# Optimization experiments

Hardware: AMD Instinct MI355X
Metric: run time of the kernel (lower is better)

Reference implementation:

```python
import jax, jax.numpy as jnp
import numpy as np

VOCAB = 32000
H = 256        # d_model
L = 4096       # l_max
N = 64         # SSM state size (S4 default)
CH = 1         # channels
BATCH = 8
PAD = 0        # pad_token_id
DT_MIN, DT_MAX = 0.001, 0.1


def setup_inputs() -> dict:
    key = jax.random.key(0)
    ks = jax.random.split(key, 8)
    input_ids = jax.random.randint(ks[0], (BATCH, L), 0, VOCAB)
    embedding = (jax.random.normal(ks[1], (VOCAB, H), dtype=jnp.float32) * 0.02).at[PAD].set(0.0)
    # S4D-Lin style initialization
    log_dt = jnp.log(DT_MIN) + jax.random.uniform(ks[2], (H,), dtype=jnp.float32) * (np.log(DT_MAX) - np.log(DT_MIN))
    A_log_re = jnp.full((H, N), np.log(0.5), dtype=jnp.float32)          # A_real = -exp(A_log_re)
    A_im = jnp.broadcast_to(np.pi * jnp.arange(N, dtype=jnp.float32), (H, N)).copy()
    B_re = jnp.ones((H, N), dtype=jnp.float32)
    B_im = jnp.zeros((H, N), dtype=jnp.float32)
    # bidirectional => 2*CH output channels for C
    C_re = jax.random.normal(ks[3], (2 * CH, H, N), dtype=jnp.float32) * (0.5 ** 0.5)
    C_im = jax.random.normal(ks[4], (2 * CH, H, N), dtype=jnp.float32) * (0.5 ** 0.5)
    D = jax.random.normal(ks[5], (CH, H), dtype=jnp.float32)
    W_out = jax.random.normal(ks[6], (2 * H, CH * H), dtype=jnp.float32) / np.sqrt(CH * H)
    b_out = jnp.zeros((2 * H,), dtype=jnp.float32)
    return {"input_ids": input_ids, "embedding": embedding, "log_dt": log_dt,
            "A_log_re": A_log_re, "A_im": A_im, "B_re": B_re, "B_im": B_im,
            "C_re": C_re, "C_im": C_im, "D": D, "W_out": W_out, "b_out": b_out}


def _s4_forward(input_ids, embedding, log_dt, A_log_re, A_im, B_re, B_im, C_re, C_im, D, W_out, b_out):
    u = embedding[input_ids]                 # (B, L, H) embedding lookup
    u = jnp.swapaxes(u, 1, 2)                # (B, H, L) transposed=True
    dt = jnp.exp(log_dt)                     # (H,)
    A = -jnp.exp(A_log_re) + 1j * A_im       # (H, N) Hurwitz diagonal SSM
    dtA = dt[:, None] * A                    # (H, N)
    dA = jnp.exp(dtA)                        # discrete A (ZOH)
    dB = (B_re + 1j * B_im) * (dA - 1.0) / A # discrete B (ZOH), (H, N)
    Cc = C_re + 1j * C_im                    # (2*CH, H, N)
    # Vandermonde kernel: K[c,h,l] = 2*Re(sum_n C[c,h,n] dB[h,n] exp(dtA[h,n]*l))
    pos = jnp.arange(L, dtype=jnp.float32)
    vand = jnp.exp(dtA[:, :, None] * pos)    # (H, N, L) complex
    K = 2.0 * jnp.einsum('chn,hn,hnl->chl', Cc, dB, vand).real  # (2*CH, H, L)
    # bidirectional: causal kernel + flipped anti-causal kernel, conv length 2L
    k0, k1 = K[:CH], K[CH:]
    k = jnp.pad(k0, ((0, 0), (0, 0), (0, L))) + jnp.pad(k1[..., ::-1], ((0, 0), (0, 0), (L, 0)))
    k_f = jnp.fft.rfft(k, n=2 * L)           # (CH, H, L+1)
    u_f = jnp.fft.rfft(u, n=2 * L)           # (B, H, L+1)
    y = jnp.fft.irfft(u_f[:, None] * k_f[None], n=2 * L)[..., :L]  # (B, CH, H, L)
    y = y + u[:, None, :, :] * D[None, :, :, None]                 # skip connection
    y = y.reshape(u.shape[0], CH * H, L)
    y = jax.nn.gelu(y, approximate=False)
    z = jnp.einsum('oi,bil->bol', W_out, y) + b_out[None, :, None]  # (B, 2H, L)
    y = z[:, :H] * jax.nn.sigmoid(z[:, H:])                          # GLU
    y = jnp.swapaxes(y, 1, 2)                # (B, L, H)
    return y[:, -1]                           # pool='last' -> (B, H)


def reference(input_ids, embedding, log_dt, A_log_re, A_im, B_re, B_im, C_re, C_im, D, W_out, b_out):
    return _s4_forward(input_ids, embedding, log_dt, A_log_re, A_im, B_re, B_im, C_re, C_im, D, W_out, b_out)
```

## Files before the change

kernel.cpp:

```cpp
#include <hip/hip_runtime.h>
#include <math.h>

#define HH 256
#define NN 64
#define LL 4096
#define BB 8
#define CC 8
#define LC (LL / CC)
#define GG 16
#define HN (HH * NN)

typedef __attribute__((ext_vector_type(2))) float pf2;
typedef __attribute__((ext_vector_type(16))) float f16v;
typedef const __attribute__((address_space(4))) f16v* cf16p;


__global__ __launch_bounds__(512) void frontend_kernel(
    const int* __restrict__ ids, const float* __restrict__ emb,
    const float* __restrict__ log_dt, const float* __restrict__ A_log_re,
    const float* __restrict__ A_im, const float* __restrict__ B_re,
    const float* __restrict__ B_im, const float* __restrict__ C_re,
    const float* __restrict__ C_im,
    float2* __restrict__ dAo, float2* __restrict__ wo, float2* __restrict__ pw,
    float* __restrict__ u_ws) {
    int t = threadIdx.x;
    if (blockIdx.x < BB * 64) {
        __shared__ int ids_s[64];
        __shared__ float tb[2][64][65];
        int b = blockIdx.x >> 6;
        int tile = blockIdx.x & 63;
        int w = t >> 6;
        int lane = t & 63;
        int rq = lane >> 4;
        int k = lane & 15;
        if (t < 64) ids_s[t] = ids[b * LL + tile * 64 + t];
        __syncthreads();
        {
            int r0 = w * 8 + rq;
            float4 v0 = *(const float4*)(emb + (long)ids_s[r0] * HH + 4 * k);
            float4 v1 = *(const float4*)(emb + (long)ids_s[r0 + 4] * HH + 4 * k);
            tb[0][r0][4 * k + 0] = v0.x;
            tb[0][r0][4 * k + 1] = v0.y;
            tb[0][r0][4 * k + 2] = v0.z;
            tb[0][r0][4 * k + 3] = v0.w;
            tb[0][r0 + 4][4 * k + 0] = v1.x;
            tb[0][r0 + 4][4 * k + 1] = v1.y;
            tb[0][r0 + 4][4 * k + 2] = v1.z;
            tb[0][r0 + 4][4 * k + 3] = v1.w;
        }
        __syncthreads();
        #pragma unroll
        for (int c4 = 0; c4 < 4; ++c4) {
            int cur = c4 & 1;
            float4 v0, v1;
            if (c4 < 3) {
                int r0 = w * 8 + rq;
                v0 = *(const float4*)(emb + (long)ids_s[r0] * HH +
                                      (c4 + 1) * 64 + 4 * k);
                v1 = *(const float4*)(emb + (long)ids_s[r0 + 4] * HH +
                                      (c4 + 1) * 64 + 4 * k);
            }
            #pragma unroll
            for (int it = 0; it < 2; ++it) {
                int hq = w * 8 + it * 4 + rq;
                int s0 = 4 * k;
                float4 o;
                o.x = tb[cur][s0 + 0][hq];
                o.y = tb[cur][s0 + 1][hq];
                o.z = tb[cur][s0 + 2][hq];
                o.w = tb[cur][s0 + 3][hq];
                *(float4*)(u_ws + ((long)(b * HH + c4 * 64 + hq)) * LL +
                           tile * 64 + s0) = o;
            }
            if (c4 < 3) {
                int r0 = w * 8 + rq;
                tb[cur ^ 1][r0][4 * k + 0] = v0.x;
                tb[cur ^ 1][r0][4 * k + 1] = v0.y;
                tb[cur ^ 1][r0][4 * k + 2] = v0.z;
                tb[cur ^ 1][r0][4 * k + 3] = v0.w;
                tb[cur ^ 1][r0 + 4][4 * k + 0] = v1.x;
                tb[cur ^ 1][r0 + 4][4 * k + 1] = v1.y;
                tb[cur ^ 1][r0 + 4][4 * k + 2] = v1.z;
                tb[cur ^ 1][r0 + 4][4 * k + 3] = v1.w;
            }
            __syncthreads();
        }
    } else {
        int idx = (blockIdx.x - BB * 64) * 512 + t;
        int h = idx >> 6;
        float dt = expf(log_dt[h]);
        float Are = -expf(A_log_re[idx]);
        float Aim = A_im[idx];
        float ea = expf(dt * Are);
        float sn, cs;
        sincosf(dt * Aim, &sn, &cs);
        float dAre = ea * cs, dAim = ea * sn;
        float numre = dAre - 1.0f, numim = dAim;
        float den = Are * Are + Aim * Aim;
        float qre = (numre * Are + numim * Aim) / den;
        float qim = (numim * Are - numre * Aim) / den;
        float bre = B_re[idx], bim = B_im[idx];
        float dBre = bre * qre - bim * qim;
        float dBim = bre * qim + bim * qre;
        float cre = C_re[idx], cim = C_im[idx];
        dAo[idx] = make_float2(dAre, dAim);
        wo[idx] = make_float2(2.0f * (cre * dBre - cim * dBim),
                              2.0f * (cre * dBim + cim * dBre));
        float pr = dAre, pi = dAim;
        #pragma unroll
        for (int kk = 0; kk < 9; ++kk) {
            float nr = pr * pr - pi * pi;
            float ni = 2.0f * pr * pi;
            pr = nr; pi = ni;
        }
        float qr = 1.0f, qi = 0.0f;
        #pragma unroll
        for (int kk = 0; kk < CC; ++kk) {
            pw[kk * HN + idx] = make_float2(qr, qi);
            float nr = qr * pr - qi * pi, ni = qr * pi + qi * pr;
            qr = nr; qi = ni;
        }
    }
}

__global__ __launch_bounds__(512) void scan_kernel(
    const float* __restrict__ u_ws, const float2* __restrict__ dAv,
    const float2* __restrict__ pw, const float2* __restrict__ wv,
    const float* __restrict__ D, float* __restrict__ g) {
    __shared__ float2 part[CC][NN];
    int t = threadIdx.x;
    int c = __builtin_amdgcn_readfirstlane(t >> 6);
    int n = t & 63;
    int bh = blockIdx.x;
    int h = bh & (HH - 1);

    float2 dA = dAv[h * NN + n];
    pf2 Q[GG];
    pf2 q; q.x = 1.0f; q.y = 0.0f;
    #pragma unroll
    for (int k = 0; k < GG; ++k) {
        Q[GG - 1 - k] = q;
        pf2 nq;
        nq.x = q.x * dA.x - q.y * dA.y;
        nq.y = q.x * dA.y + q.y * dA.x;
        q = nq;
    }
    pf2 Rp; Rp.x = q.x; Rp.y = q.x;
    pf2 Rm; Rm.x = -q.y; Rm.y = q.y;

    cf16p src = (cf16p)(unsigned long long)(u_ws + bh * LL + c * LC);
    pf2 P; P.x = 0.0f; P.y = 0.0f;
    #pragma unroll 4
    for (int j = 0; j < LC / GG; ++j) {
        f16v u = src[j];
        pf2 T; T.x = 0.0f; T.y = 0.0f;
        #pragma unroll
        for (int k = 0; k < GG; ++k) {
            pf2 ub; ub.x = u[k]; ub.y = u[k];
            T = __builtin_elementwise_fma(ub, Q[k], T);
        }
        pf2 Ps; Ps.x = P.y; Ps.y = P.x;
        P = __builtin_elementwise_fma(P, Rp, __builtin_elementwise_fma(Ps, Rm, T));
    }
    float2 sc = pw[(CC - 1 - c) * HN + h * NN + n];
    part[c][n] = make_float2(P.x * sc.x - P.y * sc.y,
                             P.x * sc.y + P.y * sc.x);
    __syncthreads();

    if (c == 0) {
        float Sr = 0.0f, Si = 0.0f;
        #pragma unroll
        for (int cc = 0; cc < CC; ++cc) {
            float2 v = part[cc][n];
            Sr += v.x; Si += v.y;
        }
        float2 wc = wv[h * NN + n];
        float contrib = fmaf(wc.x, Sr, -(wc.y * Si));
        #pragma unroll
        for (int m = 32; m > 0; m >>= 1) contrib += __shfl_xor(contrib, m);
        if (n == 0) {
            float y = contrib + u_ws[bh * LL + LL - 1] * D[h];
            float ge = 0.5f * y * (1.0f + erff(y * 0.70710678118654752f));
            g[bh] = ge;
        }
    }
}

__global__ __launch_bounds__(256) void out_kernel(
    const float* __restrict__ g, const float* __restrict__ W,
    const float* __restrict__ bvec, float* __restrict__ out) {
    int b = blockIdx.x >> 7;
    int tile = blockIdx.x & 127;
    int t = threadIdx.x;
    int w = t >> 6, lane = t & 63;
    __shared__ float gs[HH];
    __shared__ float zb[4];
    gs[t] = g[b * HH + t];
    __syncthreads();
    int hh = tile * 2 + (w >> 1);
    int o = (w & 1) * HH + hh;
    float4 wv4 = ((const float4*)(W + o * HH))[lane];
    float4 gv4 = ((const float4*)gs)[lane];
    float p = wv4.x * gv4.x + wv4.y * gv4.y + wv4.z * gv4.z + wv4.w * gv4.w;
    #pragma unroll
    for (int m = 32; m > 0; m >>= 1) p += __shfl_xor(p, m);
    if (lane == 0) zb[w] = p + bvec[o];
    __syncthreads();
    if (t < 2) {
        int hq = tile * 2 + t;
        float z1 = zb[t * 2 + 0];
        float z2 = zb[t * 2 + 1];
        out[b * HH + hq] = z1 * (1.0f / (1.0f + expf(-z2)));
    }
}

extern "C" void kernel_launch(void* const* d_in, const int* in_sizes, int n_in,
                              void* d_out, int out_size, void* d_ws, size_t ws_size,
                              hipStream_t stream) {
    const int* input_ids = (const int*)d_in[0];
    const float* embedding = (const float*)d_in[1];
    const float* log_dt = (const float*)d_in[2];
    const float* A_log_re = (const float*)d_in[3];
    const float* A_im = (const float*)d_in[4];
    const float* B_re = (const float*)d_in[5];
    const float* B_im = (const float*)d_in[6];
    const float* C_re = (const float*)d_in[7];
    const float* C_im = (const float*)d_in[8];
    const float* D = (const float*)d_in[9];
    const float* W_out = (const float*)d_in[10];
    const float* b_out = (const float*)d_in[11];
    float* out = (float*)d_out;

    float* ws = (float*)d_ws;
    float2* dAv = (float2*)ws;
    float2* wv = (float2*)(ws + 32768);
    float2* pw = (float2*)(ws + 65536);
    float* u_ws = ws + 327680;
    float* g = ws + 10813440;

    frontend_kernel<<<BB * 64 + HN / 512, 512, 0, stream>>>(
        input_ids, embedding, log_dt, A_log_re, A_im, B_re, B_im, C_re, C_im,
        dAv, wv, pw, u_ws);

    scan_kernel<<<BB * HH, 512, 0, stream>>>(u_ws, dAv, pw, wv, D, g);

    out_kernel<<<BB * 128, 256, 0, stream>>>(g, W_out, b_out, out);
}
```

Measured before the change: 134.4 us.

## Fuse three kernels into one cooperative kernel with grid syncs

Merges the embedding-transpose front end, the chunked SSM scan and the output GLU projection into one persistent cooperative kernel of 512 blocks, separated by grid-wide syncs. The SSM parameter discretisation and chunk-power scaling are now recomputed inside the scan stage, so the intermediate dA/w/pw buffers and their global round trips go away. Each block handles four (batch, head) units in sequence instead of one per block. This removes kernel launch gaps but adds grid barrier cost, and it may lose parallelism in the scan phase, which now runs fewer concurrent blocks.

```diff
diff --git a/kernel.cpp b/kernel.cpp
--- a/kernel.cpp
+++ b/kernel.cpp
@@ -1,5 +1,8 @@
 #include <hip/hip_runtime.h>
+#include <hip/hip_cooperative_groups.h>
 #include <math.h>
+
+namespace cg = cooperative_groups;
 
 #define HH 256
 #define NN 64
@@ -9,44 +12,50 @@
 #define LC (LL / CC)
 #define GG 16
 #define HN (HH * NN)
+#define GRID 512
 
 typedef __attribute__((ext_vector_type(2))) float pf2;
 typedef __attribute__((ext_vector_type(16))) float f16v;
 typedef const __attribute__((address_space(4))) f16v* cf16p;
 
-
-__global__ __launch_bounds__(512) void frontend_kernel(
+__global__ __launch_bounds__(512, 4) void fused_kernel(
     const int* __restrict__ ids, const float* __restrict__ emb,
     const float* __restrict__ log_dt, const float* __restrict__ A_log_re,
     const float* __restrict__ A_im, const float* __restrict__ B_re,
     const float* __restrict__ B_im, const float* __restrict__ C_re,
-    const float* __restrict__ C_im,
-    float2* __restrict__ dAo, float2* __restrict__ wo, float2* __restrict__ pw,
-    float* __restrict__ u_ws) {
+    const float* __restrict__ C_im, const float* __restrict__ Dv,
+    const float* __restrict__ W, const float* __restrict__ bvec,
+    float* __restrict__ u_ws, float* __restrict__ g, float* __restrict__ out) {
+    __shared__ union SMem {
+        struct { int ids_s[64]; float tb[2][64][65]; } a;
+        float2 part[CC][NN];
+        struct { float gs[HH]; float zb[8]; } o;
+    } sm;
+
     int t = threadIdx.x;
-    if (blockIdx.x < BB * 64) {
-        __shared__ int ids_s[64];
-        __shared__ float tb[2][64][65];
-        int b = blockIdx.x >> 6;
-        int tile = blockIdx.x & 63;
+    int bid = blockIdx.x;
+
+    {
+        int b = bid >> 6;
+        int tile = bid & 63;
         int w = t >> 6;
         int lane = t & 63;
         int rq = lane >> 4;
-        int k = lane & 15;
-        if (t < 64) ids_s[t] = ids[b * LL + tile * 64 + t];
+        int kc = lane & 15;
+        if (t < 64) sm.a.ids_s[t] = ids[b * LL + tile * 64 + t];
         __syncthreads();
         {
             int r0 = w * 8 + rq;
-            float4 v0 = *(const float4*)(emb + (long)ids_s[r0] * HH + 4 * k);
-            float4 v1 = *(const float4*)(emb + (long)ids_s[r0 + 4] * HH + 4 * k);
-            tb[0][r0][4 * k + 0] = v0.x;
-            tb[0][r0][4 * k + 1] = v0.y;
-            tb[0][r0][4 * k + 2] = v0.z;
-            tb[0][r0][4 * k + 3] = v0.w;
-            tb[0][r0 + 4][4 * k + 0] = v1.x;
-            tb[0][r0 + 4][4 * k + 1] = v1.y;
-            tb[0][r0 + 4][4 * k + 2] = v1.z;
-            tb[0][r0 + 4][4 * k + 3] = v1.w;
+            float4 v0 = *(const float4*)(emb + (long)sm.a.ids_s[r0] * HH + 4 * kc);
+            float4 v1 = *(const float4*)(emb + (long)sm.a.ids_s[r0 + 4] * HH + 4 * kc);
+            sm.a.tb[0][r0][4 * kc + 0] = v0.x;
+            sm.a.tb[0][r0][4 * kc + 1] = v0.y;
+            sm.a.tb[0][r0][4 * kc + 2] = v0.z;
+            sm.a.tb[0][r0][4 * kc + 3] = v0.w;
+            sm.a.tb[0][r0 + 4][4 * kc + 0] = v1.x;
+            sm.a.tb[0][r0 + 4][4 * kc + 1] = v1.y;
+            sm.a.tb[0][r0 + 4][4 * kc + 2] = v1.z;
+            sm.a.tb[0][r0 + 4][4 * kc + 3] = v1.w;
         }
         __syncthreads();
         #pragma unroll
@@ -55,162 +64,166 @@
             float4 v0, v1;
             if (c4 < 3) {
                 int r0 = w * 8 + rq;
-                v0 = *(const float4*)(emb + (long)ids_s[r0] * HH +
-                                      (c4 + 1) * 64 + 4 * k);
-                v1 = *(const float4*)(emb + (long)ids_s[r0 + 4] * HH +
-                                      (c4 + 1) * 64 + 4 * k);
+                v0 = *(const float4*)(emb + (long)sm.a.ids_s[r0] * HH +
+                                      (c4 + 1) * 64 + 4 * kc);
+                v1 = *(const float4*)(emb + (long)sm.a.ids_s[r0 + 4] * HH +
+                                      (c4 + 1) * 64 + 4 * kc);
             }
             #pragma unroll
             for (int it = 0; it < 2; ++it) {
                 int hq = w * 8 + it * 4 + rq;
-                int s0 = 4 * k;
-                float4 o;
-                o.x = tb[cur][s0 + 0][hq];
-                o.y = tb[cur][s0 + 1][hq];
-                o.z = tb[cur][s0 + 2][hq];
-                o.w = tb[cur][s0 + 3][hq];
+                int s0 = 4 * kc;
+                float4 o4;
+                o4.x = sm.a.tb[cur][s0 + 0][hq];
+                o4.y = sm.a.tb[cur][s0 + 1][hq];
+                o4.z = sm.a.tb[cur][s0 + 2][hq];
+                o4.w = sm.a.tb[cur][s0 + 3][hq];
                 *(float4*)(u_ws + ((long)(b * HH + c4 * 64 + hq)) * LL +
-                           tile * 64 + s0) = o;
+                           tile * 64 + s0) = o4;
             }
             if (c4 < 3) {
                 int r0 = w * 8 + rq;
-                tb[cur ^ 1][r0][4 * k + 0] = v0.x;
-                tb[cur ^ 1][r0][4 * k + 1] = v0.y;
-                tb[cur ^ 1][r0][4 * k + 2] = v0.z;
-                tb[cur ^ 1][r0][4 * k + 3] = v0.w;
-                tb[cur ^ 1][r0 + 4][4 * k + 0] = v1.x;
-                tb[cur ^ 1][r0 + 4][4 * k + 1] = v1.y;
-                tb[cur ^ 1][r0 + 4][4 * k + 2] = v1.z;
-                tb[cur ^ 1][r0 + 4][4 * k + 3] = v1.w;
+                sm.a.tb[cur ^ 1][r0][4 * kc + 0] = v0.x;
+                sm.a.tb[cur ^ 1][r0][4 * kc + 1] = v0.y;
+                sm.a.tb[cur ^ 1][r0][4 * kc + 2] = v0.z;
+                sm.a.tb[cur ^ 1][r0][4 * kc + 3] = v0.w;
+                sm.a.tb[cur ^ 1][r0 + 4][4 * kc + 0] = v1.x;
+                sm.a.tb[cur ^ 1][r0 + 4][4 * kc + 1] = v1.y;
+                sm.a.tb[cur ^ 1][r0 + 4][4 * kc + 2] = v1.z;
+                sm.a.tb[cur ^ 1][r0 + 4][4 * kc + 3] = v1.w;
             }
             __syncthreads();
         }
-    } else {
-        int idx = (blockIdx.x - BB * 64) * 512 + t;
-        int h = idx >> 6;
-        float dt = expf(log_dt[h]);
-        float Are = -expf(A_log_re[idx]);
-        float Aim = A_im[idx];
-        float ea = expf(dt * Are);
-        float sn, cs;
-        sincosf(dt * Aim, &sn, &cs);
-        float dAre = ea * cs, dAim = ea * sn;
-        float numre = dAre - 1.0f, numim = dAim;
-        float den = Are * Are + Aim * Aim;
-        float qre = (numre * Are + numim * Aim) / den;
-        float qim = (numim * Are - numre * Aim) / den;
-        float bre = B_re[idx], bim = B_im[idx];
-        float dBre = bre * qre - bim * qim;
-        float dBim = bre * qim + bim * qre;
-        float cre = C_re[idx], cim = C_im[idx];
-        dAo[idx] = make_float2(dAre, dAim);
-        wo[idx] = make_float2(2.0f * (cre * dBre - cim * dBim),
-                              2.0f * (cre * dBim + cim * dBre));
-        float pr = dAre, pi = dAim;
+    }
+
+    __threadfence();
+    cg::this_grid().sync();
+
+    {
+        int c = __builtin_amdgcn_readfirstlane(t >> 6);
+        int n = t & 63;
+        for (int iu = 0; iu < 4; ++iu) {
+            int unit = bid * 4 + iu;
+            int h = unit & (HH - 1);
+            int idx = h * NN + n;
+
+            float dAre, dAim, wre, wim;
+            {
+                float dt = expf(log_dt[h]);
+                float Are = -expf(A_log_re[idx]);
+                float Aim = A_im[idx];
+                float ea = expf(dt * Are);
+                float sn, cs;
+                sincosf(dt * Aim, &sn, &cs);
+                dAre = ea * cs; dAim = ea * sn;
+                float numre = dAre - 1.0f, numim = dAim;
+                float den = Are * Are + Aim * Aim;
+                float qre = (numre * Are + numim * Aim) / den;
+                float qim = (numim * Are - numre * Aim) / den;
+                float bre = B_re[idx], bim = B_im[idx];
+                float dBre = bre * qre - bim * qim;
+                float dBim = bre * qim + bim * qre;
+                float cre = C_re[idx], cim = C_im[idx];
+                wre = 2.0f * (cre * dBre - cim * dBim);
+                wim = 2.0f * (cre * dBim + cim * dBre);
+            }
+
+            pf2 Q[GG];
+            pf2 q; q.x = 1.0f; q.y = 0.0f;
+            #pragma unroll
+            for (int kk = 0; kk < GG; ++kk) {
+                Q[GG - 1 - kk] = q;
+                pf2 nq;
+                nq.x = q.x * dAre - q.y * dAim;
+                nq.y = q.x * dAim + q.y * dAre;
+                q = nq;
+            }
+            pf2 Rp; Rp.x = q.x; Rp.y = q.x;
+            pf2 Rm; Rm.x = -q.y; Rm.y = q.y;
+
+            float pr = dAre, pi = dAim;
+            #pragma unroll
+            for (int kk = 0; kk < 9; ++kk) {
+                float nr = pr * pr - pi * pi;
+                float ni = 2.0f * pr * pi;
+                pr = nr; pi = ni;
+            }
+            int e = (CC - 1) - c;
+            float sr = 1.0f, si = 0.0f;
+            #pragma unroll
+            for (int bit = 0; bit < 3; ++bit) {
+                if (e & (1 << bit)) {
+                    float nr = sr * pr - si * pi;
+                    float ni = sr * pi + si * pr;
+                    sr = nr; si = ni;
+                }
+                float nr = pr * pr - pi * pi;
+                float ni = 2.0f * pr * pi;
+                pr = nr; pi = ni;
+            }
+
+            cf16p src = (cf16p)(unsigned long long)(u_ws + (long)unit * LL + c * LC);
+            pf2 P; P.x = 0.0f; P.y = 0.0f;
+            #pragma unroll 4
+            for (int j = 0; j < LC / GG; ++j) {
+                f16v u = src[j];
+                pf2 T; T.x = 0.0f; T.y = 0.0f;
+                #pragma unroll
+                for (int kk = 0; kk < GG; ++kk) {
+                    pf2 ub; ub.x = u[kk]; ub.y = u[kk];
+                    T = __builtin_elementwise_fma(ub, Q[kk], T);
+                }
+                pf2 Ps; Ps.x = P.y; Ps.y = P.x;
+                P = __builtin_elementwise_fma(P, Rp,
+                        __builtin_elementwise_fma(Ps, Rm, T));
+            }
+            sm.part[c][n] = make_float2(P.x * sr - P.y * si,
+                                        P.x * si + P.y * sr);
+            __syncthreads();
+
+            if (c == 0) {
+                float Sr = 0.0f, Si = 0.0f;
+                #pragma unroll
+                for (int cc = 0; cc < CC; ++cc) {
+                    float2 v = sm.part[cc][n];
+                    Sr += v.x; Si += v.y;
+                }
+                float contrib = fmaf(wre, Sr, -(wim * Si));
+                #pragma unroll
+                for (int m = 32; m > 0; m >>= 1) contrib += __shfl_xor(contrib, m);
+                if (n == 0) {
+                    float y = contrib + u_ws[(long)unit * LL + LL - 1] * Dv[h];
+                    float ge = 0.5f * y * (1.0f + erff(y * 0.70710678118654752f));
+                    g[unit] = ge;
+                }
+            }
+            __syncthreads();
+        }
+    }
+
+    __threadfence();
+    cg::this_grid().sync();
+
+    {
+        int b = bid >> 6;
+        int tile = bid & 63;
+        int w = t >> 6, lane = t & 63;
+        if (t < HH) sm.o.gs[t] = g[b * HH + t];
+        __syncthreads();
+        int hh = tile * 4 + (w >> 1);
+        int o = (w & 1) * HH + hh;
+        float4 wv4 = ((const float4*)(W + o * HH))[lane];
+        float4 gv4 = ((const float4*)sm.o.gs)[lane];
+        float p = wv4.x * gv4.x + wv4.y * gv4.y + wv4.z * gv4.z + wv4.w * gv4.w;
         #pragma unroll
-        for (int kk = 0; kk < 9; ++kk) {
-            float nr = pr * pr - pi * pi;
-            float ni = 2.0f * pr * pi;
-            pr = nr; pi = ni;
-        }
-        float qr = 1.0f, qi = 0.0f;
-        #pragma unroll
-        for (int kk = 0; kk < CC; ++kk) {
-            pw[kk * HN + idx] = make_float2(qr, qi);
-            float nr = qr * pr - qi * pi, ni = qr * pi + qi * pr;
-            qr = nr; qi = ni;
-        }
-    }
-}
-
-__global__ __launch_bounds__(512) void scan_kernel(
-    const float* __restrict__ u_ws, const float2* __restrict__ dAv,
-    const float2* __restrict__ pw, const float2* __restrict__ wv,
-    const float* __restrict__ D, float* __restrict__ g) {
-    __shared__ float2 part[CC][NN];
-    int t = threadIdx.x;
-    int c = __builtin_amdgcn_readfirstlane(t >> 6);
-    int n = t & 63;
-    int bh = blockIdx.x;
-    int h = bh & (HH - 1);
-
-    float2 dA = dAv[h * NN + n];
-    pf2 Q[GG];
-    pf2 q; q.x = 1.0f; q.y = 0.0f;
-    #pragma unroll
-    for (int k = 0; k < GG; ++k) {
-        Q[GG - 1 - k] = q;
-        pf2 nq;
-        nq.x = q.x * dA.x - q.y * dA.y;
-        nq.y = q.x * dA.y + q.y * dA.x;
-        q = nq;
-    }
-    pf2 Rp; Rp.x = q.x; Rp.y = q.x;
-    pf2 Rm; Rm.x = -q.y; Rm.y = q.y;
-
-    cf16p src = (cf16p)(unsigned long long)(u_ws + bh * LL + c * LC);
-    pf2 P; P.x = 0.0f; P.y = 0.0f;
-    #pragma unroll 4
-    for (int j = 0; j < LC / GG; ++j) {
-        f16v u = src[j];
-        pf2 T; T.x = 0.0f; T.y = 0.0f;
-        #pragma unroll
-        for (int k = 0; k < GG; ++k) {
-            pf2 ub; ub.x = u[k]; ub.y = u[k];
-            T = __builtin_elementwise_fma(ub, Q[k], T);
-        }
-        pf2 Ps; Ps.x = P.y; Ps.y = P.x;
-        P = __builtin_elementwise_fma(P, Rp, __builtin_elementwise_fma(Ps, Rm, T));
-    }
-    float2 sc = pw[(CC - 1 - c) * HN + h * NN + n];
-    part[c][n] = make_float2(P.x * sc.x - P.y * sc.y,
-                             P.x * sc.y + P.y * sc.x);
-    __syncthreads();
-
-    if (c == 0) {
-        float Sr = 0.0f, Si = 0.0f;
-        #pragma unroll
-        for (int cc = 0; cc < CC; ++cc) {
-            float2 v = part[cc][n];
-            Sr += v.x; Si += v.y;
-        }
-        float2 wc = wv[h * NN + n];
-        float contrib = fmaf(wc.x, Sr, -(wc.y * Si));
-        #pragma unroll
-        for (int m = 32; m > 0; m >>= 1) contrib += __shfl_xor(contrib, m);
-        if (n == 0) {
-            float y = contrib + u_ws[bh * LL + LL - 1] * D[h];
-            float ge = 0.5f * y * (1.0f + erff(y * 0.70710678118654752f));
-            g[bh] = ge;
-        }
-    }
-}
-
-__global__ __launch_bounds__(256) void out_kernel(
-    const float* __restrict__ g, const float* __restrict__ W,
-    const float* __restrict__ bvec, float* __restrict__ out) {
-    int b = blockIdx.x >> 7;
-    int tile = blockIdx.x & 127;
-    int t = threadIdx.x;
-    int w = t >> 6, lane = t & 63;
-    __shared__ float gs[HH];
-    __shared__ float zb[4];
-    gs[t] = g[b * HH + t];
-    __syncthreads();
-    int hh = tile * 2 + (w >> 1);
-    int o = (w & 1) * HH + hh;
-    float4 wv4 = ((const float4*)(W + o * HH))[lane];
-    float4 gv4 = ((const float4*)gs)[lane];
-    float p = wv4.x * gv4.x + wv4.y * gv4.y + wv4.z * gv4.z + wv4.w * gv4.w;
-    #pragma unroll
-    for (int m = 32; m > 0; m >>= 1) p += __shfl_xor(p, m);
-    if (lane == 0) zb[w] = p + bvec[o];
-    __syncthreads();
-    if (t < 2) {
-        int hq = tile * 2 + t;
-        float z1 = zb[t * 2 + 0];
-        float z2 = zb[t * 2 + 1];
-        out[b * HH + hq] = z1 * (1.0f / (1.0f + expf(-z2)));
+        for (int m = 32; m > 0; m >>= 1) p += __shfl_xor(p, m);
+        if (lane == 0) sm.o.zb[w] = p + bvec[o];
+        __syncthreads();
+        if (t < 4) {
+            float z1 = sm.o.zb[2 * t + 0];
+            float z2 = sm.o.zb[2 * t + 1];
+            out[b * HH + tile * 4 + t] = z1 * (1.0f / (1.0f + expf(-z2)));
+        }
     }
 }
 
@@ -232,17 +245,15 @@
     float* out = (float*)d_out;
 
     float* ws = (float*)d_ws;
-    float2* dAv = (float2*)ws;
-    float2* wv = (float2*)(ws + 32768);
-    float2* pw = (float2*)(ws + 65536);
-    float* u_ws = ws + 327680;
-    float* g = ws + 10813440;
-
-    frontend_kernel<<<BB * 64 + HN / 512, 512, 0, stream>>>(
-        input_ids, embedding, log_dt, A_log_re, A_im, B_re, B_im, C_re, C_im,
-        dAv, wv, pw, u_ws);
-
-    scan_kernel<<<BB * HH, 512, 0, stream>>>(u_ws, dAv, pw, wv, D, g);
-
-    out_kernel<<<BB * 128, 256, 0, stream>>>(g, W_out, b_out, out);
+    float* u_ws = ws;
+    float* g = ws + 8388608;
+
+    void* args[] = {
+        (void*)&input_ids, (void*)&embedding, (void*)&log_dt, (void*)&A_log_re,
+        (void*)&A_im, (void*)&B_re, (void*)&B_im, (void*)&C_re, (void*)&C_im,
+        (void*)&D, (void*)&W_out, (void*)&b_out,
+        (void*)&u_ws, (void*)&g, (void*)&out
+    };
+    hipLaunchCooperativeKernel((void*)fused_kernel, dim3(GRID), dim3(512),
+                               args, 0, stream);
 }
```

Result: slower. 427.5 us (+218.0%).

## Fuse output projection into scan kernel via atomic ticket and last-block finishers

Applied to the files above, without the earlier changes.

Removes the separate out_kernel launch. Each scan block atomically stores its gelu value and takes a ticket. The last 64 blocks to arrive become finishers: they spin until all units are done, then compute the W_out projection and GLU for one batch slice. This trades a kernel launch boundary for spin-wait synchronisation and a serialized tail on a few blocks. It relies on the finisher blocks never deadlocking, which holds because they are the last to arrive and only wait on blocks that already incremented the ticket.

```diff
diff --git a/kernel.cpp b/kernel.cpp
--- a/kernel.cpp
+++ b/kernel.cpp
@@ -9,6 +9,8 @@
 #define LC (LL / CC)
 #define GG 16
 #define HN (HH * NN)
+#define UNITS (BB * HH)
+#define NFIN 64
 
 typedef __attribute__((ext_vector_type(2))) float pf2;
 typedef __attribute__((ext_vector_type(16))) float f16v;
@@ -22,7 +24,7 @@
     const float* __restrict__ B_im, const float* __restrict__ C_re,
     const float* __restrict__ C_im,
     float2* __restrict__ dAo, float2* __restrict__ wo, float2* __restrict__ pw,
-    float* __restrict__ u_ws) {
+    float* __restrict__ u_ws, int* __restrict__ ticket) {
     int t = threadIdx.x;
     if (blockIdx.x < BB * 64) {
         __shared__ int ids_s[64];
@@ -86,6 +88,7 @@
             __syncthreads();
         }
     } else {
+        if (blockIdx.x == BB * 64 && t == 0) *ticket = 0;
         int idx = (blockIdx.x - BB * 64) * 512 + t;
         int h = idx >> 6;
         float dt = expf(log_dt[h]);
@@ -126,8 +129,13 @@
 __global__ __launch_bounds__(512) void scan_kernel(
     const float* __restrict__ u_ws, const float2* __restrict__ dAv,
     const float2* __restrict__ pw, const float2* __restrict__ wv,
-    const float* __restrict__ D, float* __restrict__ g) {
+    const float* __restrict__ Dv, float* __restrict__ g,
+    const float* __restrict__ W, const float* __restrict__ bvec,
+    float* __restrict__ out, int* __restrict__ ticket) {
     __shared__ float2 part[CC][NN];
+    __shared__ int sm_role;
+    __shared__ float sm_gs[HH];
+    __shared__ float sm_zv[NFIN];
     int t = threadIdx.x;
     int c = __builtin_amdgcn_readfirstlane(t >> 6);
     int n = t & 63;
@@ -179,38 +187,48 @@
         #pragma unroll
         for (int m = 32; m > 0; m >>= 1) contrib += __shfl_xor(contrib, m);
         if (n == 0) {
-            float y = contrib + u_ws[bh * LL + LL - 1] * D[h];
+            float y = contrib + u_ws[bh * LL + LL - 1] * Dv[h];
             float ge = 0.5f * y * (1.0f + erff(y * 0.70710678118654752f));
-            g[bh] = ge;
-        }
-    }
-}
-
-__global__ __launch_bounds__(256) void out_kernel(
-    const float* __restrict__ g, const float* __restrict__ W,
-    const float* __restrict__ bvec, float* __restrict__ out) {
-    int b = blockIdx.x >> 7;
-    int tile = blockIdx.x & 127;
-    int t = threadIdx.x;
+            __hip_atomic_store(&g[bh], ge, __ATOMIC_RELEASE,
+                               __HIP_MEMORY_SCOPE_AGENT);
+            int old = __hip_atomic_fetch_add(ticket, 1, __ATOMIC_ACQ_REL,
+                                             __HIP_MEMORY_SCOPE_AGENT);
+            sm_role = old - (UNITS - NFIN);
+        }
+    }
+    __syncthreads();
+    int f = sm_role;
+    if (f < 0) return;
+
+    if (t == 0) {
+        while (__hip_atomic_load(ticket, __ATOMIC_ACQUIRE,
+                                 __HIP_MEMORY_SCOPE_AGENT) < UNITS)
+            __builtin_amdgcn_s_sleep(8);
+    }
+    __syncthreads();
+    int b = f >> 3;
+    int slice = (f & 7) * 32;
+    if (t < HH)
+        sm_gs[t] = __hip_atomic_load(&g[b * HH + t], __ATOMIC_RELAXED,
+                                     __HIP_MEMORY_SCOPE_AGENT);
+    __syncthreads();
     int w = t >> 6, lane = t & 63;
-    __shared__ float gs[HH];
-    __shared__ float zb[4];
-    gs[t] = g[b * HH + t];
-    __syncthreads();
-    int hh = tile * 2 + (w >> 1);
-    int o = (w & 1) * HH + hh;
-    float4 wv4 = ((const float4*)(W + o * HH))[lane];
-    float4 gv4 = ((const float4*)gs)[lane];
-    float p = wv4.x * gv4.x + wv4.y * gv4.y + wv4.z * gv4.z + wv4.w * gv4.w;
     #pragma unroll
-    for (int m = 32; m > 0; m >>= 1) p += __shfl_xor(p, m);
-    if (lane == 0) zb[w] = p + bvec[o];
-    __syncthreads();
-    if (t < 2) {
-        int hq = tile * 2 + t;
-        float z1 = zb[t * 2 + 0];
-        float z2 = zb[t * 2 + 1];
-        out[b * HH + hq] = z1 * (1.0f / (1.0f + expf(-z2)));
+    for (int p = 0; p < 8; ++p) {
+        int d = p * 8 + w;
+        int o = (d < 32) ? (slice + d) : (HH + slice + d - 32);
+        float4 wv4 = ((const float4*)(W + o * HH))[lane];
+        float4 gv4 = ((const float4*)sm_gs)[lane];
+        float pp = wv4.x * gv4.x + wv4.y * gv4.y + wv4.z * gv4.z + wv4.w * gv4.w;
+        #pragma unroll
+        for (int m = 32; m > 0; m >>= 1) pp += __shfl_xor(pp, m);
+        if (lane == 0) sm_zv[d] = pp + bvec[o];
+    }
+    __syncthreads();
+    if (t < 32) {
+        float z1 = sm_zv[t];
+        float z2 = sm_zv[t + 32];
+        out[b * HH + slice + t] = z1 * (1.0f / (1.0f + expf(-z2)));
     }
 }
 
@@ -237,12 +255,12 @@
     float2* pw = (float2*)(ws + 65536);
     float* u_ws = ws + 327680;
     float* g = ws + 10813440;
+    int* ticket = (int*)(ws + 10815488);
 
     frontend_kernel<<<BB * 64 + HN / 512, 512, 0, stream>>>(
         input_ids, embedding, log_dt, A_log_re, A_im, B_re, B_im, C_re, C_im,
-        dAv, wv, pw, u_ws);
-
-    scan_kernel<<<BB * HH, 512, 0, stream>>>(u_ws, dAv, pw, wv, D, g);
-
-    out_kernel<<<BB * 128, 256, 0, stream>>>(g, W_out, b_out, out);
+        dAv, wv, pw, u_ws, ticket);
+
+    scan_kernel<<<UNITS, 512, 0, stream>>>(u_ws, dAv, pw, wv, D, g,
+                                           W_out, b_out, out, ticket);
 }
```

Result: slower. 225.4 us (+67.7%).

## Materialize the SSM convolution kernel once, then dot it with inputs per batch

Applied to the files above, without the earlier changes.

Replaces the per-(batch,h) complex recurrence over 64 states with a precomputed real kernel K[h,l], built once per channel in the frontend blocks through powers of dA and shared-memory atomics. It is stored reversed, so the last output reduces to a plain dot product of u with Krev. This removes the N-fold complex work from the batch-dependent path and cuts it to 4096 FMAs per (b,h). The cost is extra kernel-building work inside the frontend blocks and roughly 4 MB of additional workspace traffic for K.

```diff
diff --git a/kernel.cpp b/kernel.cpp
--- a/kernel.cpp
+++ b/kernel.cpp
@@ -5,14 +5,6 @@
 #define NN 64
 #define LL 4096
 #define BB 8
-#define CC 8
-#define LC (LL / CC)
-#define GG 16
-#define HN (HH * NN)
-
-typedef __attribute__((ext_vector_type(2))) float pf2;
-typedef __attribute__((ext_vector_type(16))) float f16v;
-typedef const __attribute__((address_space(4))) f16v* cf16p;
 
 
 __global__ __launch_bounds__(512) void frontend_kernel(
@@ -21,32 +13,33 @@
     const float* __restrict__ A_im, const float* __restrict__ B_re,
     const float* __restrict__ B_im, const float* __restrict__ C_re,
     const float* __restrict__ C_im,
-    float2* __restrict__ dAo, float2* __restrict__ wo, float2* __restrict__ pw,
-    float* __restrict__ u_ws) {
+    float* __restrict__ u_ws, float* __restrict__ Krev) {
+    __shared__ union {
+        struct { int ids_s[64]; float tb[2][64][65]; } a;
+        struct { float4 cs4[NN]; float2 cs2[NN]; float Kbuf[LL]; } k;
+    } sm;
     int t = threadIdx.x;
     if (blockIdx.x < BB * 64) {
-        __shared__ int ids_s[64];
-        __shared__ float tb[2][64][65];
         int b = blockIdx.x >> 6;
         int tile = blockIdx.x & 63;
         int w = t >> 6;
         int lane = t & 63;
         int rq = lane >> 4;
         int k = lane & 15;
-        if (t < 64) ids_s[t] = ids[b * LL + tile * 64 + t];
+        if (t < 64) sm.a.ids_s[t] = ids[b * LL + tile * 64 + t];
         __syncthreads();
         {
             int r0 = w * 8 + rq;
-            float4 v0 = *(const float4*)(emb + (long)ids_s[r0] * HH + 4 * k);
-            float4 v1 = *(const float4*)(emb + (long)ids_s[r0 + 4] * HH + 4 * k);
-            tb[0][r0][4 * k + 0] = v0.x;
-            tb[0][r0][4 * k + 1] = v0.y;
-            tb[0][r0][4 * k + 2] = v0.z;
-            tb[0][r0][4 * k + 3] = v0.w;
-            tb[0][r0 + 4][4 * k + 0] = v1.x;
-            tb[0][r0 + 4][4 * k + 1] = v1.y;
-            tb[0][r0 + 4][4 * k + 2] = v1.z;
-            tb[0][r0 + 4][4 * k + 3] = v1.w;
+            float4 v0 = *(const float4*)(emb + (long)sm.a.ids_s[r0] * HH + 4 * k);
+            float4 v1 = *(const float4*)(emb + (long)sm.a.ids_s[r0 + 4] * HH + 4 * k);
+            sm.a.tb[0][r0][4 * k + 0] = v0.x;
+            sm.a.tb[0][r0][4 * k + 1] = v0.y;
+            sm.a.tb[0][r0][4 * k + 2] = v0.z;
+            sm.a.tb[0][r0][4 * k + 3] = v0.w;
+            sm.a.tb[0][r0 + 4][4 * k + 0] = v1.x;
+            sm.a.tb[0][r0 + 4][4 * k + 1] = v1.y;
+            sm.a.tb[0][r0 + 4][4 * k + 2] = v1.z;
+            sm.a.tb[0][r0 + 4][4 * k + 3] = v1.w;
         }
         __syncthreads();
         #pragma unroll
@@ -55,9 +48,9 @@
             float4 v0, v1;
             if (c4 < 3) {
                 int r0 = w * 8 + rq;
-                v0 = *(const float4*)(emb + (long)ids_s[r0] * HH +
+                v0 = *(const float4*)(emb + (long)sm.a.ids_s[r0] * HH +
                                       (c4 + 1) * 64 + 4 * k);
-                v1 = *(const float4*)(emb + (long)ids_s[r0 + 4] * HH +
+                v1 = *(const float4*)(emb + (long)sm.a.ids_s[r0 + 4] * HH +
                                       (c4 + 1) * 64 + 4 * k);
             }
             #pragma unroll
@@ -65,124 +58,126 @@
                 int hq = w * 8 + it * 4 + rq;
                 int s0 = 4 * k;
                 float4 o;
-                o.x = tb[cur][s0 + 0][hq];
-                o.y = tb[cur][s0 + 1][hq];
-                o.z = tb[cur][s0 + 2][hq];
-                o.w = tb[cur][s0 + 3][hq];
+                o.x = sm.a.tb[cur][s0 + 0][hq];
+                o.y = sm.a.tb[cur][s0 + 1][hq];
+                o.z = sm.a.tb[cur][s0 + 2][hq];
+                o.w = sm.a.tb[cur][s0 + 3][hq];
                 *(float4*)(u_ws + ((long)(b * HH + c4 * 64 + hq)) * LL +
                            tile * 64 + s0) = o;
             }
             if (c4 < 3) {
                 int r0 = w * 8 + rq;
-                tb[cur ^ 1][r0][4 * k + 0] = v0.x;
-                tb[cur ^ 1][r0][4 * k + 1] = v0.y;
-                tb[cur ^ 1][r0][4 * k + 2] = v0.z;
-                tb[cur ^ 1][r0][4 * k + 3] = v0.w;
-                tb[cur ^ 1][r0 + 4][4 * k + 0] = v1.x;
-                tb[cur ^ 1][r0 + 4][4 * k + 1] = v1.y;
-                tb[cur ^ 1][r0 + 4][4 * k + 2] = v1.z;
-                tb[cur ^ 1][r0 + 4][4 * k + 3] = v1.w;
+                sm.a.tb[cur ^ 1][r0][4 * k + 0] = v0.x;
+                sm.a.tb[cur ^ 1][r0][4 * k + 1] = v0.y;
+                sm.a.tb[cur ^ 1][r0][4 * k + 2] = v0.z;
+                sm.a.tb[cur ^ 1][r0][4 * k + 3] = v0.w;
+                sm.a.tb[cur ^ 1][r0 + 4][4 * k + 0] = v1.x;
+                sm.a.tb[cur ^ 1][r0 + 4][4 * k + 1] = v1.y;
+                sm.a.tb[cur ^ 1][r0 + 4][4 * k + 2] = v1.z;
+                sm.a.tb[cur ^ 1][r0 + 4][4 * k + 3] = v1.w;
             }
             __syncthreads();
         }
     } else {
-        int idx = (blockIdx.x - BB * 64) * 512 + t;
-        int h = idx >> 6;
-        float dt = expf(log_dt[h]);
-        float Are = -expf(A_log_re[idx]);
-        float Aim = A_im[idx];
-        float ea = expf(dt * Are);
-        float sn, cs;
-        sincosf(dt * Aim, &sn, &cs);
-        float dAre = ea * cs, dAim = ea * sn;
-        float numre = dAre - 1.0f, numim = dAim;
-        float den = Are * Are + Aim * Aim;
-        float qre = (numre * Are + numim * Aim) / den;
-        float qim = (numim * Are - numre * Aim) / den;
-        float bre = B_re[idx], bim = B_im[idx];
-        float dBre = bre * qre - bim * qim;
-        float dBim = bre * qim + bim * qre;
-        float cre = C_re[idx], cim = C_im[idx];
-        dAo[idx] = make_float2(dAre, dAim);
-        wo[idx] = make_float2(2.0f * (cre * dBre - cim * dBim),
-                              2.0f * (cre * dBim + cim * dBre));
-        float pr = dAre, pi = dAim;
-        #pragma unroll
-        for (int kk = 0; kk < 9; ++kk) {
-            float nr = pr * pr - pi * pi;
-            float ni = 2.0f * pr * pi;
-            pr = nr; pi = ni;
-        }
-        float qr = 1.0f, qi = 0.0f;
-        #pragma unroll
-        for (int kk = 0; kk < CC; ++kk) {
-            pw[kk * HN + idx] = make_float2(qr, qi);
-            float nr = qr * pr - qi * pi, ni = qr * pi + qi * pr;
-            qr = nr; qi = ni;
-        }
-    }
-}
-
-__global__ __launch_bounds__(512) void scan_kernel(
-    const float* __restrict__ u_ws, const float2* __restrict__ dAv,
-    const float2* __restrict__ pw, const float2* __restrict__ wv,
-    const float* __restrict__ D, float* __restrict__ g) {
-    __shared__ float2 part[CC][NN];
+        int h = blockIdx.x - BB * 64;
+        int w = t >> 6, lane = t & 63;
+        #pragma unroll
+        for (int i = 0; i < 8; ++i) sm.k.Kbuf[i * 512 + t] = 0.0f;
+        if (t < NN) {
+            int n = t;
+            int idx = h * NN + n;
+            float dt = expf(log_dt[h]);
+            float Are = -expf(A_log_re[idx]);
+            float Aim = A_im[idx];
+            float ea = expf(dt * Are);
+            float sn, cs;
+            sincosf(dt * Aim, &sn, &cs);
+            float dAre = ea * cs, dAim = ea * sn;
+            float numre = dAre - 1.0f, numim = dAim;
+            float den = Are * Are + Aim * Aim;
+            float qre = (numre * Are + numim * Aim) / den;
+            float qim = (numim * Are - numre * Aim) / den;
+            float bre = B_re[idx], bim = B_im[idx];
+            float dBre = bre * qre - bim * qim;
+            float dBim = bre * qim + bim * qre;
+            float cre = C_re[idx], cim = C_im[idx];
+            float wre = 2.0f * (cre * dBre - cim * dBim);
+            float wim = 2.0f * (cre * dBim + cim * dBre);
+            float pr = dAre, pi = dAim;
+            #pragma unroll
+            for (int kq = 0; kq < 6; ++kq) {
+                float nr = pr * pr - pi * pi;
+                pi = 2.0f * pr * pi; pr = nr;
+            }
+            sm.k.cs4[n] = make_float4(dAre, dAim, wre, wim);
+            sm.k.cs2[n] = make_float2(pr, pi);
+        }
+        __syncthreads();
+        float kacc[64];
+        #pragma unroll
+        for (int j = 0; j < 64; ++j) kacc[j] = 0.0f;
+        #pragma unroll 2
+        for (int nn = 0; nn < 8; ++nn) {
+            int n = w * 8 + nn;
+            float4 c4 = sm.k.cs4[n];
+            float2 c2 = sm.k.cs2[n];
+            float pr = 1.0f, pi = 0.0f, br = c4.x, bi = c4.y;
+            #pragma unroll
+            for (int bit = 0; bit < 6; ++bit) {
+                bool on = (lane >> bit) & 1;
+                float mr = on ? br : 1.0f;
+                float mi = on ? bi : 0.0f;
+                float tr = pr * mr - pi * mi;
+                pi = pr * mi + pi * mr; pr = tr;
+                float t2 = br * br - bi * bi;
+                bi = 2.0f * br * bi; br = t2;
+            }
+            float vr = c4.z * pr - c4.w * pi;
+            float vi = c4.z * pi + c4.w * pr;
+            #pragma unroll
+            for (int j = 0; j < 64; ++j) {
+                kacc[j] += vr;
+                float tr = vr * c2.x - vi * c2.y;
+                vi = vr * c2.y + vi * c2.x; vr = tr;
+            }
+        }
+        #pragma unroll
+        for (int j = 0; j < 64; ++j)
+            atomicAdd(&sm.k.Kbuf[j * 64 + lane], kacc[j]);
+        __syncthreads();
+        #pragma unroll
+        for (int i = 0; i < 8; ++i) {
+            int tp = i * 512 + t;
+            Krev[h * LL + tp] = sm.k.Kbuf[LL - 1 - tp];
+        }
+    }
+}
+
+__global__ __launch_bounds__(256) void conv_kernel(
+    const float* __restrict__ u_ws, const float* __restrict__ Krev,
+    const float* __restrict__ Dv, float* __restrict__ g) {
+    __shared__ float partial[4];
     int t = threadIdx.x;
-    int c = __builtin_amdgcn_readfirstlane(t >> 6);
-    int n = t & 63;
     int bh = blockIdx.x;
     int h = bh & (HH - 1);
-
-    float2 dA = dAv[h * NN + n];
-    pf2 Q[GG];
-    pf2 q; q.x = 1.0f; q.y = 0.0f;
+    const float4* up = (const float4*)(u_ws + (long)bh * LL);
+    const float4* kp = (const float4*)(Krev + h * LL);
+    float acc = 0.0f;
     #pragma unroll
-    for (int k = 0; k < GG; ++k) {
-        Q[GG - 1 - k] = q;
-        pf2 nq;
-        nq.x = q.x * dA.x - q.y * dA.y;
-        nq.y = q.x * dA.y + q.y * dA.x;
-        q = nq;
-    }
-    pf2 Rp; Rp.x = q.x; Rp.y = q.x;
-    pf2 Rm; Rm.x = -q.y; Rm.y = q.y;
-
-    cf16p src = (cf16p)(unsigned long long)(u_ws + bh * LL + c * LC);
-    pf2 P; P.x = 0.0f; P.y = 0.0f;
-    #pragma unroll 4
-    for (int j = 0; j < LC / GG; ++j) {
-        f16v u = src[j];
-        pf2 T; T.x = 0.0f; T.y = 0.0f;
-        #pragma unroll
-        for (int k = 0; k < GG; ++k) {
-            pf2 ub; ub.x = u[k]; ub.y = u[k];
-            T = __builtin_elementwise_fma(ub, Q[k], T);
-        }
-        pf2 Ps; Ps.x = P.y; Ps.y = P.x;
-        P = __builtin_elementwise_fma(P, Rp, __builtin_elementwise_fma(Ps, Rm, T));
-    }
-    float2 sc = pw[(CC - 1 - c) * HN + h * NN + n];
-    part[c][n] = make_float2(P.x * sc.x - P.y * sc.y,
-                             P.x * sc.y + P.y * sc.x);
+    for (int i = 0; i < 4; ++i) {
+        float4 uv = up[i * 256 + t];
+        float4 kv = kp[i * 256 + t];
+        acc += uv.x * kv.x + uv.y * kv.y + uv.z * kv.z + uv.w * kv.w;
+    }
+    #pragma unroll
+    for (int m = 32; m > 0; m >>= 1) acc += __shfl_xor(acc, m);
+    if ((t & 63) == 0) partial[t >> 6] = acc;
     __syncthreads();
-
-    if (c == 0) {
-        float Sr = 0.0f, Si = 0.0f;
-        #pragma unroll
-        for (int cc = 0; cc < CC; ++cc) {
-            float2 v = part[cc][n];
-            Sr += v.x; Si += v.y;
-        }
-        float2 wc = wv[h * NN + n];
-        float contrib = fmaf(wc.x, Sr, -(wc.y * Si));
-        #pragma unroll
-        for (int m = 32; m > 0; m >>= 1) contrib += __shfl_xor(contrib, m);
-        if (n == 0) {
-            float y = contrib + u_ws[bh * LL + LL - 1] * D[h];
-            float ge = 0.5f * y * (1.0f + erff(y * 0.70710678118654752f));
-            g[bh] = ge;
-        }
+    if (t == 0) {
+        float y = partial[0] + partial[1] + partial[2] + partial[3]
+                + u_ws[(long)bh * LL + LL - 1] * Dv[h];
+        float ge = 0.5f * y * (1.0f + erff(y * 0.70710678118654752f));
+        g[bh] = ge;
     }
 }
 
@@ -232,17 +227,15 @@
     float* out = (float*)d_out;
 
     float* ws = (float*)d_ws;
-    float2* dAv = (float2*)ws;
-    float2* wv = (float2*)(ws + 32768);
-    float2* pw = (float2*)(ws + 65536);
     float* u_ws = ws + 327680;
     float* g = ws + 10813440;
-
-    frontend_kernel<<<BB * 64 + HN / 512, 512, 0, stream>>>(
+    float* Krev = ws + 10815488;
+
+    frontend_kernel<<<BB * 64 + HH, 512, 0, stream>>>(
         input_ids, embedding, log_dt, A_log_re, A_im, B_re, B_im, C_re, C_im,
-        dAv, wv, pw, u_ws);
-
-    scan_kernel<<<BB * HH, 512, 0, stream>>>(u_ws, dAv, pw, wv, D, g);
+        u_ws, Krev);
+
+    conv_kernel<<<BB * HH, 256, 0, stream>>>(u_ws, Krev, D, g);
 
     out_kernel<<<BB * 128, 256, 0, stream>>>(g, W_out, b_out, out);
 }
```

Result: slower. 211.4 us (+57.3%).
